# Kernel tuning notes

Measured on AMD Instinct MI355X. Metric: run time of the kernel, lower is better.

The kernel has to match this reference:

```python
import jax, jax.numpy as jnp
import numpy as np

N = 50000      # nodes
E = 800000     # edges
F_IN = 256     # num_n_feature
EMB = 128      # emb_size
GF = 32        # num_g_feature
G = 256        # graphs in batch
NEG_SLOPE = 0.2


def setup_inputs() -> dict:
    key = jax.random.key(0)
    ks = jax.random.split(key, 20)
    p = lambda i, shape: (jax.random.normal(ks[i], shape, jnp.float32) * 0.05)
    return {
        "x": jax.random.normal(ks[0], (N, F_IN), jnp.float32),
        "edges_idx": jax.random.randint(ks[1], (2, E), 0, N, dtype=jnp.int32),
        "batch_idx": jnp.sort(jax.random.randint(ks[2], (N,), 0, G, dtype=jnp.int32)),
        "g_features": jax.random.normal(ks[3], (G, GF), jnp.float32),
        # GATConv 1
        "W1": p(4, (F_IN, EMB)), "a1_src": p(5, (EMB,)), "a1_dst": p(6, (EMB,)), "b1": p(7, (EMB,)),
        # GATConv 2
        "W2": p(8, (EMB, EMB)), "a2_src": p(9, (EMB,)), "a2_dst": p(10, (EMB,)), "b2": p(11, (EMB,)),
        # lin_g
        "Wg": p(12, (GF, EMB)), "bg": p(13, (EMB,)),
        # out head: Linear(3*emb, 2)
        "Wo": p(14, (3 * EMB, 2)), "bo": p(15, (2,)),
    }


def gat_conv(x, src, dst, W, a_src, a_dst, b, n):
    """PyG GATConv, heads=1, with self-loops; attention dropout omitted (eval)."""
    h = x @ W                                  # [N, emb]
    loop = jnp.arange(n, dtype=src.dtype)
    src = jnp.concatenate([src, loop])         # add self loops
    dst = jnp.concatenate([dst, loop])
    e = jax.nn.leaky_relu((h @ a_src)[src] + (h @ a_dst)[dst], NEG_SLOPE)  # [E+N]
    # segment softmax over destination nodes
    m = jax.lax.stop_gradient(jax.ops.segment_max(e, dst, num_segments=n))
    m = jnp.where(jnp.isfinite(m), m, 0.0)
    p = jnp.exp(e - m[dst])
    den = jax.ops.segment_sum(p, dst, num_segments=n)
    alpha = p / den[dst]
    out = jax.ops.segment_sum(alpha[:, None] * h[src], dst, num_segments=n)
    return out + b


def reference(x, edges_idx, batch_idx, g_features,
              W1, a1_src, a1_dst, b1, W2, a2_src, a2_dst, b2,
              Wg, bg, Wo, bo):
    src, dst = edges_idx[0], edges_idx[1]
    h = gat_conv(x, src, dst, W1, a1_src, a1_dst, b1, N)
    h = gat_conv(h, src, dst, W2, a2_src, a2_dst, b2, N)
    # global mean / max pooling per graph
    counts = jax.ops.segment_sum(jnp.ones((N,), h.dtype), batch_idx, num_segments=G)
    mean = jax.ops.segment_sum(h, batch_idx, num_segments=G) / jnp.maximum(counts, 1.0)[:, None]
    mx = jax.ops.segment_max(h, batch_idx, num_segments=G)
    mx = jnp.where(jnp.isfinite(mx), mx, 0.0)
    g_ft = g_features @ Wg + bg
    flat = jnp.concatenate([mean, mx, g_ft], axis=1)   # [G, 3*emb]
    return jax.nn.log_softmax(flat @ Wo + bo, axis=-1)  # [G, 2]
```

## Files before the change

### kernel.cpp

```cpp
#include <hip/hip_runtime.h>
#include <hip/hip_bf16.h>

#define N_NODES 50000
#define N_EDGES 800000
#define FIN 256
#define EMB 128
#define NGRAPH 256
#define TOT_E (N_EDGES + N_NODES)
#define NP 98
#define RBLK 196
#define NB 391

typedef __bf16 bf16;
typedef __attribute__((ext_vector_type(8))) __bf16 bf16x8;
typedef __attribute__((ext_vector_type(4))) __bf16 bf16x4;
typedef __attribute__((ext_vector_type(2))) __bf16 bf16x2;
typedef __attribute__((ext_vector_type(4))) float f32x4;
typedef __attribute__((ext_vector_type(4))) int i32x4;

__global__ void transpose_kernel(const float* __restrict__ src, bf16* __restrict__ dst,
                                 int rows, int cols) {
    int t = blockIdx.x * 256 + threadIdx.x;
    if (t >= rows * cols) return;
    int c = t / rows, r = t - c * rows;
    dst[t] = (bf16)src[r * cols + c];
}

__global__ __launch_bounds__(256)
void hist_part_kernel(const int* __restrict__ e_dst, int* __restrict__ counts,
                      int* __restrict__ mat) {
    __shared__ int lh[NP];
    int t = threadIdx.x;
    for (int k = t; k < NP; k += 256) lh[k] = 0;
    __syncthreads();
    const int NQ = N_EDGES / 4;
    int base = blockIdx.x * 1024;
#pragma unroll
    for (int j = 0; j < 4; ++j) {
        int i = base + j * 256 + t;
        if (i < NQ) {
            i32x4 d4 = *(const i32x4*)(e_dst + 4 * i);
#pragma unroll
            for (int k = 0; k < 4; ++k) {
                atomicAdd(&counts[d4[k]], 1);
                atomicAdd(&lh[d4[k] >> 9], 1);
            }
        }
    }
    __syncthreads();
    for (int k = t; k < NP; k += 256) mat[k * RBLK + blockIdx.x] = lh[k];
}

__global__ __launch_bounds__(1024)
void scan_block_kernel(const int* __restrict__ counts, int* __restrict__ offsets,
                       int* __restrict__ blocksums) {
    __shared__ int lds[1024];
    int t = threadIdx.x;
    int idx = blockIdx.x * 1024 + t;
    int v = (idx < N_NODES) ? counts[idx] + 1 : 0;
    lds[t] = v;
    __syncthreads();
    for (int d = 1; d < 1024; d <<= 1) {
        int u = (t >= d) ? lds[t - d] : 0;
        __syncthreads();
        lds[t] += u;
        __syncthreads();
    }
    if (idx < N_NODES) offsets[idx] = lds[t] - v;
    if (t == 1023) blocksums[blockIdx.x] = lds[1023];
}

__global__ __launch_bounds__(1024)
void scan_fix_kernel(int* __restrict__ offsets, const int* __restrict__ blocksums,
                     int nblk, int* __restrict__ sorted) {
    __shared__ int sprefix;
    int t = threadIdx.x, b = blockIdx.x;
    if (t < 64) {
        int v = (t < b && t < nblk) ? blocksums[t] : 0;
#pragma unroll
        for (int mk = 32; mk >= 1; mk >>= 1) v += __shfl_xor(v, mk);
        if (t == 0) sprefix = v;
    }
    __syncthreads();
    int idx = b * 1024 + t;
    if (idx < N_NODES) {
        int off = offsets[idx] + sprefix;
        offsets[idx] = off;
        sorted[off] = idx;
    }
    if (idx == 0) offsets[N_NODES] = TOT_E;
}

__global__ __launch_bounds__(256)
void rowscan_kernel(int* __restrict__ mat, int* __restrict__ rowsum) {
    __shared__ int lds[256];
    int p = blockIdx.x, t = threadIdx.x;
    int v = (t < RBLK) ? mat[p * RBLK + t] : 0;
    lds[t] = v;
    __syncthreads();
    for (int d = 1; d < 256; d <<= 1) {
        int u = (t >= d) ? lds[t - d] : 0;
        __syncthreads();
        lds[t] += u;
        __syncthreads();
    }
    if (t < RBLK) mat[p * RBLK + t] = lds[t] - v;
    if (t == 255) rowsum[p] = lds[255];
}

__global__ __launch_bounds__(128)
void partbase_kernel(const int* __restrict__ rowsum, int* __restrict__ poff) {
    __shared__ int lds[128];
    int t = threadIdx.x;
    int v = (t < NP) ? rowsum[t] : 0;
    lds[t] = v;
    __syncthreads();
    for (int d = 1; d < 128; d <<= 1) {
        int u = (t >= d) ? lds[t - d] : 0;
        __syncthreads();
        lds[t] += u;
        __syncthreads();
    }
    if (t < NP) poff[t] = lds[t] - v;
    if (t == 0) poff[NP] = N_EDGES;
}

__global__ __launch_bounds__(256)
void radix_scatter_kernel(const int* __restrict__ e_src, const int* __restrict__ e_dst,
                          const int* __restrict__ mat, const int* __restrict__ poff,
                          unsigned* __restrict__ pairs) {
    __shared__ int cur[NP];
    int t = threadIdx.x;
    for (int k = t; k < NP; k += 256) cur[k] = poff[k] + mat[k * RBLK + blockIdx.x];
    __syncthreads();
    const int NQ = N_EDGES / 4;
    int base = blockIdx.x * 1024;
#pragma unroll
    for (int j = 0; j < 4; ++j) {
        int i = base + j * 256 + t;
        if (i < NQ) {
            i32x4 d4 = *(const i32x4*)(e_dst + 4 * i);
            i32x4 s4 = *(const i32x4*)(e_src + 4 * i);
#pragma unroll
            for (int k = 0; k < 4; ++k) {
                int d = d4[k];
                int pos = atomicAdd(&cur[d >> 9], 1);
                pairs[pos] = ((unsigned)d << 16) | (unsigned)s4[k];
            }
        }
    }
}

__global__ __launch_bounds__(1024)
void bucket_place_kernel(const int* __restrict__ poff, const int* __restrict__ offsets,
                         const unsigned* __restrict__ pairs, int* __restrict__ sorted) {
    int b = blockIdx.x;
    int t = threadIdx.x;
    int lo = b * 128;
    __shared__ int cur[128];
    if (t < 128 && lo + t < N_NODES) cur[t] = offsets[lo + t] + 1;
    __syncthreads();
    int p = b >> 2;
    int p0 = poff[p], p1 = poff[p + 1];
    unsigned blo = (unsigned)b;
    for (int i = p0 + t; i < p1; i += 1024) {
        unsigned v = pairs[i];
        unsigned d = v >> 16;
        if ((d >> 7) == blo) {
            int pos = atomicAdd(&cur[d & 127], 1);
            sorted[pos] = (int)(v & 0xFFFFu);
        }
    }
}

template<int K, typename AT>
__global__ __launch_bounds__(256)
void gemm_kernel(const AT* __restrict__ A, const bf16* __restrict__ WT,
                 bf16* __restrict__ C, int M,
                 const float* __restrict__ a_src, const float* __restrict__ a_dst,
                 float* __restrict__ s_src, float* __restrict__ s_dst) {
    __shared__ __align__(16) bf16 As[64][64];
    __shared__ __align__(16) bf16 Bs[128][64];
    int tid = threadIdx.x;
    int wave = tid >> 6, lane = tid & 63;
    int m0 = blockIdx.x * 64;

    f32x4 acc[8];
#pragma unroll
    for (int i = 0; i < 8; ++i) acc[i] = (f32x4){0.f, 0.f, 0.f, 0.f};

    for (int k0 = 0; k0 < K; k0 += 64) {
        if constexpr (sizeof(AT) == 4) {
#pragma unroll
            for (int it = 0; it < 4; ++it) {
                int task = tid + it * 256;
                int row = task >> 4, seg4 = task & 15;
                int gr = m0 + row;
                float4 f = make_float4(0.f, 0.f, 0.f, 0.f);
                if (gr < M) f = *(const float4*)((const float*)A + (size_t)gr * K + k0 + seg4 * 4);
                bf16x4 b4 = (bf16x4){(bf16)f.x, (bf16)f.y, (bf16)f.z, (bf16)f.w};
                int slot = seg4 >> 1, half8 = seg4 & 1;
                int ss = slot ^ (row & 7);
                *(bf16x4*)(&As[row][ss * 8 + half8 * 4]) = b4;
            }
        } else {
#pragma unroll
            for (int it = 0; it < 2; ++it) {
                int task = tid + it * 256;
                int row = task >> 3, slot = task & 7;
                int gr = m0 + row;
                uint4 v = make_uint4(0u, 0u, 0u, 0u);
                if (gr < M) v = *(const uint4*)((const bf16*)A + (size_t)gr * K + k0 + slot * 8);
                int ss = slot ^ (row & 7);
                *(uint4*)(&As[row][ss * 8]) = v;
            }
        }
#pragma unroll
        for (int it = 0; it < 4; ++it) {
            int task = tid + it * 256;
            int col = task >> 3, slot = task & 7;
            uint4 v = *(const uint4*)(WT + (size_t)col * K + k0 + slot * 8);
            int ss = slot ^ (col & 7);
            *(uint4*)(&Bs[col][ss * 8]) = v;
        }
        __syncthreads();
        int r = wave * 16 + (lane & 15);
        int kk = lane >> 4;
        bf16x8 af0 = *(const bf16x8*)(&As[r][((kk) ^ (r & 7)) * 8]);
        bf16x8 af1 = *(const bf16x8*)(&As[r][((4 + kk) ^ (r & 7)) * 8]);
#pragma unroll
        for (int n = 0; n < 8; ++n) {
            int c = n * 16 + (lane & 15);
            bf16x8 b0 = *(const bf16x8*)(&Bs[c][((kk) ^ (c & 7)) * 8]);
            bf16x8 b1 = *(const bf16x8*)(&Bs[c][((4 + kk) ^ (c & 7)) * 8]);
            acc[n] = __builtin_amdgcn_mfma_f32_16x16x32_bf16(af0, b0, acc[n], 0, 0, 0);
            acc[n] = __builtin_amdgcn_mfma_f32_16x16x32_bf16(af1, b1, acc[n], 0, 0, 0);
        }
        __syncthreads();
    }
    int rbase = m0 + wave * 16 + ((lane >> 4) << 2);
    int cbase = lane & 15;
#pragma unroll
    for (int n = 0; n < 8; ++n) {
#pragma unroll
        for (int r = 0; r < 4; ++r) {
            int row = rbase + r;
            if (row < M) C[(size_t)row * 128 + n * 16 + cbase] = (bf16)acc[n][r];
        }
    }
    float a_s[8], a_d[8];
#pragma unroll
    for (int n = 0; n < 8; ++n) {
        a_s[n] = a_src[n * 16 + cbase];
        a_d[n] = a_dst[n * 16 + cbase];
    }
#pragma unroll
    for (int r = 0; r < 4; ++r) {
        float ps = 0.f, pd = 0.f;
#pragma unroll
        for (int n = 0; n < 8; ++n) {
            ps += acc[n][r] * a_s[n];
            pd += acc[n][r] * a_d[n];
        }
#pragma unroll
        for (int mk = 8; mk >= 1; mk >>= 1) {
            ps += __shfl_xor(ps, mk);
            pd += __shfl_xor(pd, mk);
        }
        int row = rbase + r;
        if (cbase == 0 && row < M) { s_src[row] = ps; s_dst[row] = pd; }
    }
}

template<typename OUT_T>
__global__ __launch_bounds__(256)
void agg_kernel(const int* __restrict__ offsets, const int* __restrict__ sorted_src,
                const float* __restrict__ s_src, const float* __restrict__ s_dst,
                const bf16* __restrict__ h, const float* __restrict__ bias,
                OUT_T* __restrict__ out) {
    int tid = threadIdx.x;
    int wave = tid >> 6, lane = tid & 63;
    int gl = lane & 15;
    int gbase = lane & 48;
    int d = blockIdx.x * 16 + wave * 4 + (lane >> 4);
    if (d >= N_NODES) return;
    int r0 = offsets[d];
    int deg = offsets[d + 1] - r0;
    float sd = s_dst[d];

    int sv0 = 0, sv1 = 0;
    float ev0 = -INFINITY, ev1 = -INFINITY;
    if (gl < deg) {
        sv0 = sorted_src[r0 + gl];
        float e = s_src[sv0] + sd;
        ev0 = (e > 0.f) ? e : 0.2f * e;
    }
    if (16 + gl < deg) {
        sv1 = sorted_src[r0 + 16 + gl];
        float e = s_src[sv1] + sd;
        ev1 = (e > 0.f) ? e : 0.2f * e;
    }
    float m = fmaxf(ev0, ev1);
    for (int i = 32 + gl; i < deg; i += 16) {
        int s = sorted_src[r0 + i];
        float e = s_src[s] + sd;
        e = (e > 0.f) ? e : 0.2f * e;
        m = fmaxf(m, e);
    }
#pragma unroll
    for (int mk = 8; mk >= 1; mk >>= 1) m = fmaxf(m, __shfl_xor(m, mk));

    float pv0 = (gl < deg) ? __expf(ev0 - m) : 0.f;
    float pv1 = (16 + gl < deg) ? __expf(ev1 - m) : 0.f;
    float den = pv0 + pv1;
    for (int i = 32 + gl; i < deg; i += 16) {
        int s = sorted_src[r0 + i];
        float e = s_src[s] + sd;
        e = (e > 0.f) ? e : 0.2f * e;
        den += __expf(e - m);
    }
#pragma unroll
    for (int mk = 8; mk >= 1; mk >>= 1) den += __shfl_xor(den, mk);

    float acc[8];
#pragma unroll
    for (int k = 0; k < 8; ++k) acc[k] = 0.f;

    int jm = (deg < 32) ? deg : 32;
#pragma unroll 4
    for (int j = 0; j < jm; ++j) {
        int src_lane = gbase + (j & 15);
        int s = __shfl((j < 16) ? sv0 : sv1, src_lane);
        float p = __shfl((j < 16) ? pv0 : pv1, src_lane);
        bf16x8 hv = *(const bf16x8*)(h + (size_t)s * 128 + gl * 8);
#pragma unroll
        for (int k = 0; k < 8; ++k) acc[k] += p * (float)hv[k];
    }
    for (int i = 32; i < deg; ++i) {
        int s = sorted_src[r0 + i];
        float e = s_src[s] + sd;
        e = (e > 0.f) ? e : 0.2f * e;
        float p = __expf(e - m);
        bf16x8 hv = *(const bf16x8*)(h + (size_t)s * 128 + gl * 8);
#pragma unroll
        for (int k = 0; k < 8; ++k) acc[k] += p * (float)hv[k];
    }

    float inv = 1.f / den;
    float4 bv0 = *(const float4*)(bias + gl * 8);
    float4 bv1 = *(const float4*)(bias + gl * 8 + 4);
    float o[8] = {acc[0] * inv + bv0.x, acc[1] * inv + bv0.y,
                  acc[2] * inv + bv0.z, acc[3] * inv + bv0.w,
                  acc[4] * inv + bv1.x, acc[5] * inv + bv1.y,
                  acc[6] * inv + bv1.z, acc[7] * inv + bv1.w};
    if constexpr (sizeof(OUT_T) == 2) {
        bf16x8 ov;
#pragma unroll
        for (int k = 0; k < 8; ++k) ov[k] = (bf16)o[k];
        *(bf16x8*)((bf16*)out + (size_t)d * 128 + gl * 8) = ov;
    } else {
        float* op = (float*)out + (size_t)d * 128 + gl * 8;
        *(float4*)op       = (float4){o[0], o[1], o[2], o[3]};
        *(float4*)(op + 4) = (float4){o[4], o[5], o[6], o[7]};
    }
}

__global__ __launch_bounds__(256)
void pool_kernel(const bf16* __restrict__ out2, const int* __restrict__ batch_idx,
                 float* __restrict__ mean, float* __restrict__ mx) {
    int g = blockIdx.x;
    int j = threadIdx.x & 127;
    int grp = threadIdx.x >> 7;
    int lo = 0, hi = N_NODES;
    while (lo < hi) { int mid = (lo + hi) >> 1; if (batch_idx[mid] < g) lo = mid + 1; else hi = mid; }
    int start = lo;
    hi = N_NODES;
    while (lo < hi) { int mid = (lo + hi) >> 1; if (batch_idx[mid] < g + 1) lo = mid + 1; else hi = mid; }
    int end = lo;

    float s = 0.f, mmax = -INFINITY;
    for (int r = start + grp; r < end; r += 2) {
        float v = (float)out2[(size_t)r * 128 + j];
        s += v;
        mmax = fmaxf(mmax, v);
    }
    __shared__ float ls[2][128], lm[2][128];
    ls[grp][j] = s; lm[grp][j] = mmax;
    __syncthreads();
    if (grp == 0) {
        int cnt = end - start;
        float sum = ls[0][j] + ls[1][j];
        float mv = fmaxf(lm[0][j], lm[1][j]);
        mean[g * 128 + j] = sum / fmaxf((float)cnt, 1.f);
        mx[g * 128 + j] = (cnt > 0) ? mv : 0.f;
    }
}

__global__ __launch_bounds__(128)
void head_kernel(const float* __restrict__ mean, const float* __restrict__ mx,
                 const float* __restrict__ gfeat, const float* __restrict__ Wg,
                 const float* __restrict__ bg, const float* __restrict__ Wo,
                 const float* __restrict__ bo, float* __restrict__ out) {
    int g = blockIdx.x;
    int j = threadIdx.x;
    float gft = bg[j];
#pragma unroll
    for (int k = 0; k < 32; ++k)
        gft += gfeat[g * 32 + k] * Wg[k * 128 + j];
    float mj = mean[g * 128 + j], xj = mx[g * 128 + j];
    float p0 = mj * Wo[j * 2 + 0] + xj * Wo[(128 + j) * 2 + 0] + gft * Wo[(256 + j) * 2 + 0];
    float p1 = mj * Wo[j * 2 + 1] + xj * Wo[(128 + j) * 2 + 1] + gft * Wo[(256 + j) * 2 + 1];
#pragma unroll
    for (int m = 32; m >= 1; m >>= 1) { p0 += __shfl_xor(p0, m); p1 += __shfl_xor(p1, m); }
    __shared__ float l0s[2], l1s[2];
    int wv = j >> 6;
    if ((j & 63) == 0) { l0s[wv] = p0; l1s[wv] = p1; }
    __syncthreads();
    if (j == 0) {
        float l0 = l0s[0] + l0s[1] + bo[0];
        float l1 = l1s[0] + l1s[1] + bo[1];
        float mm = fmaxf(l0, l1);
        float lse = mm + logf(__expf(l0 - mm) + __expf(l1 - mm));
        out[g * 2 + 0] = l0 - lse;
        out[g * 2 + 1] = l1 - lse;
    }
}

extern "C" void kernel_launch(void* const* d_in, const int* in_sizes, int n_in,
                              void* d_out, int out_size, void* d_ws, size_t ws_size,
                              hipStream_t stream) {
    const float* x     = (const float*)d_in[0];
    const int*   edges = (const int*)d_in[1];
    const int*   batch = (const int*)d_in[2];
    const float* gfeat = (const float*)d_in[3];
    const float* W1    = (const float*)d_in[4];
    const float* a1s   = (const float*)d_in[5];
    const float* a1d   = (const float*)d_in[6];
    const float* b1    = (const float*)d_in[7];
    const float* W2    = (const float*)d_in[8];
    const float* a2s   = (const float*)d_in[9];
    const float* a2d   = (const float*)d_in[10];
    const float* b2    = (const float*)d_in[11];
    const float* Wg    = (const float*)d_in[12];
    const float* bg    = (const float*)d_in[13];
    const float* Wo    = (const float*)d_in[14];
    const float* bo    = (const float*)d_in[15];

    char* ws = (char*)d_ws;
    bf16*     WT1       = (bf16*)(ws + 0);
    bf16*     WT2       = (bf16*)(ws + 65536);
    float*    s_src     = (float*)(ws + 98304);
    float*    s_dst     = (float*)(ws + 299008);
    int*      counts    = (int*)(ws + 499712);
    int*      blocksums = (int*)(ws + 700416);
    int*      mat       = (int*)(ws + 700672);
    int*      rowsum    = (int*)(ws + 777536);
    int*      poff      = (int*)(ws + 777984);
    int*      offsets   = (int*)(ws + 778432);
    int*      sorted    = (int*)(ws + 979136);
    bf16*     h         = (bf16*)(ws + 4502528);
    bf16*     out1      = (bf16*)(ws + 17302528);
    bf16*     out2      = (bf16*)(ws + 30102528);
    unsigned* pairs     = (unsigned*)(ws + 43002528);
    float*    pmean     = (float*)(ws + 55702528);
    float*    pmax      = (float*)(ws + 55833600);

    const int* e_src = edges;
    const int* e_dst = edges + N_EDGES;

    transpose_kernel<<<(FIN * EMB + 255) / 256, 256, 0, stream>>>(W1, WT1, FIN, EMB);
    transpose_kernel<<<(EMB * EMB + 255) / 256, 256, 0, stream>>>(W2, WT2, EMB, EMB);

    hipMemsetAsync(counts, 0, N_NODES * sizeof(int), stream);
    hist_part_kernel<<<RBLK, 256, 0, stream>>>(e_dst, counts, mat);
    int nblk = (N_NODES + 1023) / 1024;
    scan_block_kernel<<<nblk, 1024, 0, stream>>>(counts, offsets, blocksums);
    scan_fix_kernel<<<nblk, 1024, 0, stream>>>(offsets, blocksums, nblk, sorted);
    rowscan_kernel<<<NP, 256, 0, stream>>>(mat, rowsum);
    partbase_kernel<<<1, 128, 0, stream>>>(rowsum, poff);
    radix_scatter_kernel<<<RBLK, 256, 0, stream>>>(e_src, e_dst, mat, poff, pairs);
    bucket_place_kernel<<<NB, 1024, 0, stream>>>(poff, offsets, pairs, sorted);

    int gemm_blocks = (N_NODES + 63) / 64;
    int agg_blocks = (N_NODES + 15) / 16;

    gemm_kernel<FIN, float><<<gemm_blocks, 256, 0, stream>>>(x, WT1, h, N_NODES,
                                                             a1s, a1d, s_src, s_dst);
    agg_kernel<bf16><<<agg_blocks, 256, 0, stream>>>(offsets, sorted, s_src, s_dst, h, b1, out1);

    gemm_kernel<EMB, bf16><<<gemm_blocks, 256, 0, stream>>>(out1, WT2, h, N_NODES,
                                                            a2s, a2d, s_src, s_dst);
    agg_kernel<bf16><<<agg_blocks, 256, 0, stream>>>(offsets, sorted, s_src, s_dst, h, b2, out2);

    pool_kernel<<<NGRAPH, 256, 0, stream>>>(out2, batch, pmean, pmax);
    head_kernel<<<NGRAPH, 128, 0, stream>>>(pmean, pmax, gfeat, Wg, bg, Wo, bo, (float*)d_out);
}
```

Before: 213.4 us.

## Load GEMM operands directly from global memory, merge transposes, unroll aggregation

The GEMM kernel no longer stages A and W tiles through shared memory with barriers. Each lane now loads its MFMA fragments straight from global memory, relying on cache to serve the reused weight rows. The two weight-transpose launches are merged into one kernel, and the aggregation inner loop unroll goes from 4 to 8. This saves a launch plus LDS traffic and synchronisation, but the weight loads become uncoalesced and are repeated by every wave.

```diff
diff --git a/kernel.cpp b/kernel.cpp
--- a/kernel.cpp
+++ b/kernel.cpp
@@ -18,12 +18,17 @@
 typedef __attribute__((ext_vector_type(4))) float f32x4;
 typedef __attribute__((ext_vector_type(4))) int i32x4;
 
-__global__ void transpose_kernel(const float* __restrict__ src, bf16* __restrict__ dst,
-                                 int rows, int cols) {
+__global__ void transpose2_kernel(const float* __restrict__ W1, bf16* __restrict__ WT1,
+                                  const float* __restrict__ W2, bf16* __restrict__ WT2) {
     int t = blockIdx.x * 256 + threadIdx.x;
-    if (t >= rows * cols) return;
-    int c = t / rows, r = t - c * rows;
-    dst[t] = (bf16)src[r * cols + c];
+    if (t < FIN * EMB) {
+        int c = t / FIN, r = t - c * FIN;
+        WT1[t] = (bf16)W1[r * EMB + c];
+    } else if (t < FIN * EMB + EMB * EMB) {
+        int u = t - FIN * EMB;
+        int c = u / EMB, r = u - c * EMB;
+        WT2[u] = (bf16)W2[r * EMB + c];
+    }
 }
 
 __global__ __launch_bounds__(256)
@@ -179,73 +184,55 @@
                  bf16* __restrict__ C, int M,
                  const float* __restrict__ a_src, const float* __restrict__ a_dst,
                  float* __restrict__ s_src, float* __restrict__ s_dst) {
-    __shared__ __align__(16) bf16 As[64][64];
-    __shared__ __align__(16) bf16 Bs[128][64];
     int tid = threadIdx.x;
     int wave = tid >> 6, lane = tid & 63;
     int m0 = blockIdx.x * 64;
+    int r = m0 + wave * 16 + (lane & 15);
+    int kseg = lane >> 4;
+    bool rok = r < M;
 
     f32x4 acc[8];
 #pragma unroll
     for (int i = 0; i < 8; ++i) acc[i] = (f32x4){0.f, 0.f, 0.f, 0.f};
 
     for (int k0 = 0; k0 < K; k0 += 64) {
+        bf16x8 af0, af1;
         if constexpr (sizeof(AT) == 4) {
-#pragma unroll
-            for (int it = 0; it < 4; ++it) {
-                int task = tid + it * 256;
-                int row = task >> 4, seg4 = task & 15;
-                int gr = m0 + row;
-                float4 f = make_float4(0.f, 0.f, 0.f, 0.f);
-                if (gr < M) f = *(const float4*)((const float*)A + (size_t)gr * K + k0 + seg4 * 4);
-                bf16x4 b4 = (bf16x4){(bf16)f.x, (bf16)f.y, (bf16)f.z, (bf16)f.w};
-                int slot = seg4 >> 1, half8 = seg4 & 1;
-                int ss = slot ^ (row & 7);
-                *(bf16x4*)(&As[row][ss * 8 + half8 * 4]) = b4;
+            const float* ap = (const float*)A + (size_t)r * K + k0 + kseg * 8;
+            float4 f0 = make_float4(0.f, 0.f, 0.f, 0.f), f1 = f0, f2 = f0, f3 = f0;
+            if (rok) {
+                f0 = *(const float4*)(ap);
+                f1 = *(const float4*)(ap + 4);
+                f2 = *(const float4*)(ap + 32);
+                f3 = *(const float4*)(ap + 36);
             }
+            af0 = (bf16x8){(bf16)f0.x, (bf16)f0.y, (bf16)f0.z, (bf16)f0.w,
+                           (bf16)f1.x, (bf16)f1.y, (bf16)f1.z, (bf16)f1.w};
+            af1 = (bf16x8){(bf16)f2.x, (bf16)f2.y, (bf16)f2.z, (bf16)f2.w,
+                           (bf16)f3.x, (bf16)f3.y, (bf16)f3.z, (bf16)f3.w};
         } else {
-#pragma unroll
-            for (int it = 0; it < 2; ++it) {
-                int task = tid + it * 256;
-                int row = task >> 3, slot = task & 7;
-                int gr = m0 + row;
-                uint4 v = make_uint4(0u, 0u, 0u, 0u);
-                if (gr < M) v = *(const uint4*)((const bf16*)A + (size_t)gr * K + k0 + slot * 8);
-                int ss = slot ^ (row & 7);
-                *(uint4*)(&As[row][ss * 8]) = v;
-            }
-        }
-#pragma unroll
-        for (int it = 0; it < 4; ++it) {
-            int task = tid + it * 256;
-            int col = task >> 3, slot = task & 7;
-            uint4 v = *(const uint4*)(WT + (size_t)col * K + k0 + slot * 8);
-            int ss = slot ^ (col & 7);
-            *(uint4*)(&Bs[col][ss * 8]) = v;
-        }
-        __syncthreads();
-        int r = wave * 16 + (lane & 15);
-        int kk = lane >> 4;
-        bf16x8 af0 = *(const bf16x8*)(&As[r][((kk) ^ (r & 7)) * 8]);
-        bf16x8 af1 = *(const bf16x8*)(&As[r][((4 + kk) ^ (r & 7)) * 8]);
+            const bf16* ap = (const bf16*)A + (size_t)r * K + k0 + kseg * 8;
+            af0 = rok ? *(const bf16x8*)(ap)      : (bf16x8){0, 0, 0, 0, 0, 0, 0, 0};
+            af1 = rok ? *(const bf16x8*)(ap + 32) : (bf16x8){0, 0, 0, 0, 0, 0, 0, 0};
+        }
 #pragma unroll
         for (int n = 0; n < 8; ++n) {
             int c = n * 16 + (lane & 15);
-            bf16x8 b0 = *(const bf16x8*)(&Bs[c][((kk) ^ (c & 7)) * 8]);
-            bf16x8 b1 = *(const bf16x8*)(&Bs[c][((4 + kk) ^ (c & 7)) * 8]);
+            const bf16* bp = WT + (size_t)c * K + k0 + kseg * 8;
+            bf16x8 b0 = *(const bf16x8*)(bp);
+            bf16x8 b1 = *(const bf16x8*)(bp + 32);
             acc[n] = __builtin_amdgcn_mfma_f32_16x16x32_bf16(af0, b0, acc[n], 0, 0, 0);
             acc[n] = __builtin_amdgcn_mfma_f32_16x16x32_bf16(af1, b1, acc[n], 0, 0, 0);
         }
-        __syncthreads();
     }
     int rbase = m0 + wave * 16 + ((lane >> 4) << 2);
     int cbase = lane & 15;
 #pragma unroll
     for (int n = 0; n < 8; ++n) {
 #pragma unroll
-        for (int r = 0; r < 4; ++r) {
-            int row = rbase + r;
-            if (row < M) C[(size_t)row * 128 + n * 16 + cbase] = (bf16)acc[n][r];
+        for (int rr = 0; rr < 4; ++rr) {
+            int row = rbase + rr;
+            if (row < M) C[(size_t)row * 128 + n * 16 + cbase] = (bf16)acc[n][rr];
         }
     }
     float a_s[8], a_d[8];
@@ -255,19 +242,19 @@
         a_d[n] = a_dst[n * 16 + cbase];
     }
 #pragma unroll
-    for (int r = 0; r < 4; ++r) {
+    for (int rr = 0; rr < 4; ++rr) {
         float ps = 0.f, pd = 0.f;
 #pragma unroll
         for (int n = 0; n < 8; ++n) {
-            ps += acc[n][r] * a_s[n];
-            pd += acc[n][r] * a_d[n];
+            ps += acc[n][rr] * a_s[n];
+            pd += acc[n][rr] * a_d[n];
         }
 #pragma unroll
         for (int mk = 8; mk >= 1; mk >>= 1) {
             ps += __shfl_xor(ps, mk);
             pd += __shfl_xor(pd, mk);
         }
-        int row = rbase + r;
+        int row = rbase + rr;
         if (cbase == 0 && row < M) { s_src[row] = ps; s_dst[row] = pd; }
     }
 }
@@ -327,7 +314,7 @@
     for (int k = 0; k < 8; ++k) acc[k] = 0.f;
 
     int jm = (deg < 32) ? deg : 32;
-#pragma unroll 4
+#pragma unroll 8
     for (int j = 0; j < jm; ++j) {
         int src_lane = gbase + (j & 15);
         int s = __shfl((j < 16) ? sv0 : sv1, src_lane);
@@ -468,8 +455,7 @@
     const int* e_src = edges;
     const int* e_dst = edges + N_EDGES;
 
-    transpose_kernel<<<(FIN * EMB + 255) / 256, 256, 0, stream>>>(W1, WT1, FIN, EMB);
-    transpose_kernel<<<(EMB * EMB + 255) / 256, 256, 0, stream>>>(W2, WT2, EMB, EMB);
+    transpose2_kernel<<<(FIN * EMB + EMB * EMB + 255) / 256, 256, 0, stream>>>(W1, WT1, W2, WT2);
 
     hipMemsetAsync(counts, 0, N_NODES * sizeof(int), stream);
     hist_part_kernel<<<RBLK, 256, 0, stream>>>(e_dst, counts, mat);
```

Result: slower. 250.3 us (+17.3%).
